# Kernel tuning notes

Hardware: AMD Instinct MI355X
Metric: run time of the kernel (lower is better)

## Reference

```python
import jax, jax.numpy as jnp
import numpy as np

B, S, E, H, DK = 2, 2048, 2048, 16, 128


def _make_freq_pos_enc(dim, max_seq_len):
    # matches torch freq_pos_enc: interleaved repeat '(f r)' with r=2
    inv_freq = 1.0 / (10000.0 ** (jnp.arange(0, dim, 2, dtype=jnp.float32) / dim))
    pos = jnp.arange(max_seq_len, dtype=jnp.float32)
    pe = pos[:, None] * inv_freq[None, :]          # [S, dim/2]
    return jnp.repeat(pe, 2, axis=-1)              # [S, dim], interleaved


def setup_inputs() -> dict:
    key = jax.random.key(0)
    ks = jax.random.split(key, 5)
    sc = 1.0 / np.sqrt(E)
    return {
        "x": jax.random.normal(ks[0], (B, S, E), jnp.float32),
        "wq": jax.random.normal(ks[1], (H * DK, E), jnp.float32) * sc,
        "wk": jax.random.normal(ks[2], (H * DK, E), jnp.float32) * sc,
        "wv": jax.random.normal(ks[3], (H * DK, E), jnp.float32) * sc,
        "wo": jax.random.normal(ks[4], (E, H * DK), jnp.float32) * sc,
        "freq_pos_enc": _make_freq_pos_enc(DK, S),
        "num_heads": H,
        "d_k": DK,
    }


def rotate_half(u):
    # interleaved pairs: (d r) with r=2 -> (-u2, u1) interleaved back
    shp = u.shape
    u = u.reshape(shp[:-1] + (shp[-1] // 2, 2))
    u1, u2 = u[..., 0], u[..., 1]
    return jnp.stack((-u2, u1), axis=-1).reshape(shp)


def reference(x, wq, wk, wv, wo, freq_pos_enc, num_heads, d_k):
    b, s, _ = x.shape

    def proj(w):  # [B,S,E] @ [E, H*DK] -> [B,H,S,DK]
        return (x @ w.T).reshape(b, s, num_heads, d_k).transpose(0, 2, 1, 3)

    q, k, v = proj(wq), proj(wk), proj(wv)

    pe = freq_pos_enc[:s]                           # [S, DK]
    cos, sin = jnp.cos(pe), jnp.sin(pe)
    rot = lambda u: u * cos + rotate_half(u) * sin  # broadcast over [B,H]
    q, k = rot(q), rot(k)

    scale = 1.0 / jnp.sqrt(jnp.asarray(d_k, x.dtype))
    scores = jnp.einsum('bhqd,bhkd->bhqk', q, k) * scale
    causal = jnp.tril(jnp.ones((s, s), bool))
    scores = jnp.where(causal, scores, jnp.finfo(scores.dtype).min)
    attn = jnp.einsum('bhqk,bhkd->bhqd', jax.nn.softmax(scores, axis=-1), v)

    out = attn.transpose(0, 2, 1, 3).reshape(b, s, num_heads * d_k)
    return out @ wo.T
```

## Files before the change

kernel.cpp:

```cpp
#include <hip/hip_runtime.h>
#include <hip/hip_bf16.h>

typedef __attribute__((ext_vector_type(8))) short bf16x8;
typedef __attribute__((ext_vector_type(4))) float f32x4;
typedef unsigned short u16;
typedef unsigned int u32;

#define B_ 2
#define S_ 2048
#define E_ 2048
#define H_ 16
#define DK_ 128
#define SCALE_ 0.08838834764831845f
#define THR_RAW_ 90.5f

#define MFMA16(a,b,c) __builtin_amdgcn_mfma_f32_16x16x32_bf16((a),(b),(c),0,0,0)
#define GLD16(g, l) __builtin_amdgcn_global_load_lds((const __attribute__((address_space(1))) void*)(g), (__attribute__((address_space(3))) void*)(l), 16, 0, 0)

__device__ __forceinline__ float b2f(short s) {
    u32 u = ((u32)(u16)s) << 16;
    float f; __builtin_memcpy(&f, &u, 4); return f;
}

__global__ void cast_f32_bf16(const float* __restrict__ in, __hip_bfloat16* __restrict__ out, int n4) {
    int i = blockIdx.x * blockDim.x + threadIdx.x;
    if (i >= n4) return;
    float4 v = ((const float4*)in)[i];
    __hip_bfloat16 ob[4] = {__float2bfloat16(v.x), __float2bfloat16(v.y),
                            __float2bfloat16(v.z), __float2bfloat16(v.w)};
    ushort4 u; __builtin_memcpy(&u, ob, 8);
    ((ushort4*)out)[i] = u;
}

__global__ void rope_kernel(__hip_bfloat16* __restrict__ q, __hip_bfloat16* __restrict__ k,
                            const float* __restrict__ pe) {
    const long i = ((long)blockIdx.x * blockDim.x + threadIdx.x) * 8;
    __hip_bfloat16* p = (blockIdx.y == 0 ? q : k) + i;
    const int d0 = (int)(i & (DK_ - 1));
    const int s  = (int)((i >> 7) & (S_ - 1));
    const float* pp = pe + (size_t)s * DK_ + d0;
    bf16x8 v = *(const bf16x8*)p;
    __hip_bfloat16 ob[8];
    #pragma unroll
    for (int j = 0; j < 4; ++j) {
        float ang = pp[2*j];
        float cs = cosf(ang), sn = sinf(ang);
        float e = b2f(v[2*j]), o = b2f(v[2*j+1]);
        ob[2*j]   = __float2bfloat16(e*cs - o*sn);
        ob[2*j+1] = __float2bfloat16(o*cs + e*sn);
    }
    bf16x8 w; __builtin_memcpy(&w, ob, 16);
    *(bf16x8*)p = w;
}

template<int OUTMODE>
__global__ __launch_bounds__(256, 2)
void gemm_bt(const __hip_bfloat16* __restrict__ A, const __hip_bfloat16* __restrict__ W,
             void* __restrict__ Cout, int M, int N, int K)
{
    __shared__ __align__(16) __hip_bfloat16 As[128 * 64];
    __shared__ __align__(16) __hip_bfloat16 Bs[128 * 64];
    const int tid = threadIdx.x;
    const int lane = tid & 63, wv = tid >> 6;
    const int wr = wv >> 1, wc = wv & 1;
    const int m0 = blockIdx.x * 128, n0 = blockIdx.y * 128;
    const int g = lane >> 4, c = lane & 15;

    f32x4 acc[4][4];
    #pragma unroll
    for (int i = 0; i < 4; ++i)
        #pragma unroll
        for (int j = 0; j < 4; ++j) acc[i][j] = f32x4{0.f, 0.f, 0.f, 0.f};

    for (int k0 = 0; k0 < K; k0 += 64) {
        __syncthreads();
        #pragma unroll
        for (int it = 0; it < 4; ++it) {
            int o = (it * 256 + tid) * 16;
            int row = o >> 7;
            int colb = (o ^ ((row & 7) << 4)) & 127;
            GLD16((const char*)(A + (size_t)(m0 + row) * K + k0) + colb, (char*)As + o);
            GLD16((const char*)(W + (size_t)(n0 + row) * K + k0) + colb, (char*)Bs + o);
        }
        __syncthreads();
        #pragma unroll
        for (int ks = 0; ks < 2; ++ks) {
            bf16x8 af[4], bfm[4];
            #pragma unroll
            for (int i = 0; i < 4; ++i) {
                int arow = wr * 64 + i * 16 + c;
                int ab = arow * 128 + ((ks * 64 + g * 16) ^ ((arow & 7) << 4));
                af[i] = *(const bf16x8*)((const char*)As + ab);
                int brow = wc * 64 + i * 16 + c;
                int bb = brow * 128 + ((ks * 64 + g * 16) ^ ((brow & 7) << 4));
                bfm[i] = *(const bf16x8*)((const char*)Bs + bb);
            }
            #pragma unroll
            for (int i = 0; i < 4; ++i)
                #pragma unroll
                for (int j = 0; j < 4; ++j)
                    acc[i][j] = MFMA16(af[i], bfm[j], acc[i][j]);
        }
    }

    #pragma unroll
    for (int i = 0; i < 4; ++i) {
        #pragma unroll
        for (int j = 0; j < 4; ++j) {
            #pragma unroll
            for (int r = 0; r < 4; ++r) {
                int m = m0 + wr * 64 + i * 16 + 4 * g + r;
                int n = n0 + wc * 64 + j * 16 + c;
                float v = acc[i][j][r];
                if (OUTMODE == 2) {
                    ((float*)Cout)[(size_t)m * N + n] = v;
                } else if (OUTMODE == 0) {
                    size_t a = ((size_t)((m >> 11) * 16 + (n >> 7)) * S_ + (m & (S_ - 1))) * DK_ + (n & (DK_ - 1));
                    ((__hip_bfloat16*)Cout)[a] = __float2bfloat16(v);
                } else {
                    size_t a = ((size_t)((n >> 11) * 16 + (m >> 7)) * DK_ + (m & (DK_ - 1))) * S_ + (n & (S_ - 1));
                    ((__hip_bfloat16*)Cout)[a] = __float2bfloat16(v);
                }
            }
        }
    }
}

__device__ __forceinline__ void stage_kv(const __hip_bfloat16* Kp, const __hip_bfloat16* Vp,
                                         char* ks, char* vs, int kv0, int tid) {
    #pragma unroll
    for (int it = 0; it < 4; ++it) {
        int o = (it * 256 + tid) * 16;
        int row = o >> 8;
        int cb = (o ^ ((row & 7) << 4)) & 255;
        GLD16((const char*)(Kp + (size_t)(kv0 + row) * DK_) + cb, ks + o);
    }
    #pragma unroll
    for (int it = 0; it < 4; ++it) {
        int o = (it * 256 + tid) * 16;
        int row = o >> 7;
        int cb = (o ^ ((row & 7) << 4)) & 127;
        GLD16((const char*)(Vp + (size_t)row * S_ + kv0) + cb, vs + o);
    }
}

__global__ __launch_bounds__(256, 2)
void attn_kernel(const __hip_bfloat16* __restrict__ Q,
                 const __hip_bfloat16* __restrict__ Kt,
                 const __hip_bfloat16* __restrict__ VT,
                 __hip_bfloat16* __restrict__ O)
{
    __shared__ __align__(16) __hip_bfloat16 Ks[2][64 * 128];
    __shared__ __align__(16) __hip_bfloat16 Vs[2][128 * 64];
    __shared__ __align__(16) __hip_bfloat16 Ps[4][16 * 72];

    const int tid = threadIdx.x, lane = tid & 63, w = tid >> 6;
    const int g = lane >> 4, c = lane & 15;
    const int bh = blockIdx.y, b = bh >> 4, h = bh & 15;
    const size_t base_bh = (size_t)bh * S_ * DK_;
    const __hip_bfloat16* Qp = Q + base_bh;
    const __hip_bfloat16* Kp = Kt + base_bh;
    const __hip_bfloat16* Vp = VT + base_bh;

    #pragma unroll 1
    for (int pass = 0; pass < 2; ++pass) {
        const int qt = pass ? (31 - (int)blockIdx.x) : (int)blockIdx.x;
        const int qw = qt * 64 + w * 16;
        const int ntiles = qt + 1;

        bf16x8 qf[4];
        #pragma unroll
        for (int ds = 0; ds < 4; ++ds)
            qf[ds] = *(const bf16x8*)(Qp + (size_t)(qw + c) * DK_ + ds * 32 + g * 8);

        f32x4 oacc[8];
        #pragma unroll
        for (int fd = 0; fd < 8; ++fd) oacc[fd] = f32x4{0.f, 0.f, 0.f, 0.f};
        float M[4], L[4];
        #pragma unroll
        for (int r = 0; r < 4; ++r) { M[r] = -1e30f; L[r] = 0.f; }

        stage_kv(Kp, Vp, (char*)Ks[0], (char*)Vs[0], 0, tid);
        __syncthreads();

        int cur = 0;
        for (int t = 0; t < ntiles; ++t) {
            const int kv0 = t * 64;
            if (t + 1 < ntiles)
                stage_kv(Kp, Vp, (char*)Ks[cur ^ 1], (char*)Vs[cur ^ 1], kv0 + 64, tid);

            const bool diag = (kv0 + 63 > qw);

            f32x4 sacc[4];
            #pragma unroll
            for (int f = 0; f < 4; ++f) sacc[f] = f32x4{0.f, 0.f, 0.f, 0.f};
            #pragma unroll
            for (int f = 0; f < 4; ++f) {
                #pragma unroll
                for (int ds = 0; ds < 4; ++ds) {
                    int krow = f * 16 + c;
                    int kbyt = krow * 256 + ((ds * 64 + g * 16) ^ ((krow & 7) << 4));
                    bf16x8 kf = *(const bf16x8*)((const char*)Ks[cur] + kbyt);
                    sacc[f] = MFMA16(qf[ds], kf, sacc[f]);
                }
            }

            float p[4][4];
            float mt[4] = {-1e30f, -1e30f, -1e30f, -1e30f};
            #pragma unroll
            for (int f = 0; f < 4; ++f)
                #pragma unroll
                for (int r = 0; r < 4; ++r) {
                    float v = sacc[f][r];
                    if (diag && (kv0 + f * 16 + c > qw + 4 * g + r)) v = -1e30f;
                    p[f][r] = v;
                    mt[r] = fmaxf(mt[r], v);
                }
            #pragma unroll
            for (int r = 0; r < 4; ++r) {
                float v = mt[r];
                v = fmaxf(v, __shfl_xor(v, 1));
                v = fmaxf(v, __shfl_xor(v, 2));
                v = fmaxf(v, __shfl_xor(v, 4));
                v = fmaxf(v, __shfl_xor(v, 8));
                mt[r] = v;
            }
            bool grow = (mt[0] > M[0] + THR_RAW_) || (mt[1] > M[1] + THR_RAW_) ||
                        (mt[2] > M[2] + THR_RAW_) || (mt[3] > M[3] + THR_RAW_);
            if (__any(grow)) {
                float al[4];
                #pragma unroll
                for (int r = 0; r < 4; ++r) {
                    float mn = fmaxf(M[r], mt[r]);
                    al[r] = __expf((M[r] - mn) * SCALE_);
                    M[r] = mn;
                    L[r] *= al[r];
                }
                #pragma unroll
                for (int fd = 0; fd < 8; ++fd)
                    #pragma unroll
                    for (int r = 0; r < 4; ++r) oacc[fd][r] *= al[r];
            }
            float ms[4];
            #pragma unroll
            for (int r = 0; r < 4; ++r) ms[r] = M[r] * SCALE_;
            float lt[4] = {0.f, 0.f, 0.f, 0.f};
            #pragma unroll
            for (int f = 0; f < 4; ++f)
                #pragma unroll
                for (int r = 0; r < 4; ++r) {
                    float e = __expf(__builtin_fmaf(p[f][r], SCALE_, -ms[r]));
                    lt[r] += e;
                    Ps[w][(4 * g + r) * 72 + f * 16 + c] = __float2bfloat16(e);
                }
            #pragma unroll
            for (int r = 0; r < 4; ++r) {
                float v = lt[r];
                v += __shfl_xor(v, 1);
                v += __shfl_xor(v, 2);
                v += __shfl_xor(v, 4);
                v += __shfl_xor(v, 8);
                L[r] += v;
            }

            #pragma unroll
            for (int ks2 = 0; ks2 < 2; ++ks2) {
                bf16x8 pf = *(const bf16x8*)&Ps[w][c * 72 + ks2 * 32 + g * 8];
                #pragma unroll
                for (int fd = 0; fd < 8; ++fd) {
                    int vrow = fd * 16 + c;
                    int vb = vrow * 128 + ((ks2 * 64 + g * 16) ^ ((vrow & 7) << 4));
                    bf16x8 vf = *(const bf16x8*)((const char*)Vs[cur] + vb);
                    oacc[fd] = MFMA16(pf, vf, oacc[fd]);
                }
            }
            __syncthreads();
            cur ^= 1;
        }

        float rl[4];
        #pragma unroll
        for (int r = 0; r < 4; ++r) rl[r] = 1.0f / L[r];
        #pragma unroll
        for (int fd = 0; fd < 8; ++fd) {
            #pragma unroll
            for (int r = 0; r < 4; ++r) {
                int s = qw + 4 * g + r;
                size_t a = ((size_t)(b * S_ + s)) * (H_ * DK_) + h * DK_ + fd * 16 + c;
                O[a] = __float2bfloat16(oacc[fd][r] * rl[r]);
            }
        }
    }
}

extern "C" void kernel_launch(void* const* d_in, const int* in_sizes, int n_in,
                              void* d_out, int out_size, void* d_ws, size_t ws_size,
                              hipStream_t stream) {
    const float* x  = (const float*)d_in[0];
    const float* wq = (const float*)d_in[1];
    const float* wk = (const float*)d_in[2];
    const float* wv = (const float*)d_in[3];
    const float* wo = (const float*)d_in[4];
    const float* pe = (const float*)d_in[5];
    float* out = (float*)d_out;

    const size_t XE = (size_t)B_ * S_ * E_;
    const size_t WE = (size_t)E_ * H_ * DK_;
    __hip_bfloat16* xb  = (__hip_bfloat16*)d_ws;
    __hip_bfloat16* wqb = xb + XE;
    __hip_bfloat16* wkb = wqb + WE;
    __hip_bfloat16* wvb = wkb + WE;
    __hip_bfloat16* wob = wvb + WE;
    __hip_bfloat16* qb  = wob + WE;
    __hip_bfloat16* kb  = qb + XE;
    __hip_bfloat16* vT  = kb + XE;
    __hip_bfloat16* at  = vT + XE;

    cast_f32_bf16<<<dim3((int)(XE / 4 / 256)), 256, 0, stream>>>(x,  xb,  (int)(XE / 4));
    cast_f32_bf16<<<dim3((int)(WE / 4 / 256)), 256, 0, stream>>>(wq, wqb, (int)(WE / 4));
    cast_f32_bf16<<<dim3((int)(WE / 4 / 256)), 256, 0, stream>>>(wk, wkb, (int)(WE / 4));
    cast_f32_bf16<<<dim3((int)(WE / 4 / 256)), 256, 0, stream>>>(wv, wvb, (int)(WE / 4));
    cast_f32_bf16<<<dim3((int)(WE / 4 / 256)), 256, 0, stream>>>(wo, wob, (int)(WE / 4));

    gemm_bt<0><<<dim3(32, 16), 256, 0, stream>>>(xb, wqb, qb, B_ * S_, H_ * DK_, E_);
    gemm_bt<0><<<dim3(32, 16), 256, 0, stream>>>(xb, wkb, kb, B_ * S_, H_ * DK_, E_);
    gemm_bt<1><<<dim3(16, 32), 256, 0, stream>>>(wvb, xb, vT, H_ * DK_, B_ * S_, E_);

    rope_kernel<<<dim3((int)(XE / 8 / 256), 2), 256, 0, stream>>>(qb, kb, pe);

    attn_kernel<<<dim3(16, B_ * H_), 256, 0, stream>>>(qb, kb, vT, at);

    gemm_bt<2><<<dim3(32, 16), 256, 0, stream>>>(at, wob, out, B_ * S_, E_, H_ * DK_);
}
```

Baseline: 299.6 us.

## Fuse QKV projections with RoPE epilogue, batch weight casts, remap attention grid

Merges the three Q/K/V projection GEMMs into a single launch and applies RoPE inside the Q/K epilogue using a precomputed cos/sin table and a lane shuffle to fetch the paired element. This removes the separate rope pass over Q and K. The four weight casts become one launch, and the V transpose store is vectorised to 4-element writes. The attention grid is flattened and remapped so that groups of heads are interleaved across blocks, which may improve L2 locality or load balance. In exchange the epilogue does extra global reads of the trig table, and the output GEMM is specialised to fp32 output.

```diff
diff --git a/kernel.cpp b/kernel.cpp
--- a/kernel.cpp
+++ b/kernel.cpp
@@ -32,31 +32,128 @@
     ((ushort4*)out)[i] = u;
 }
 
-__global__ void rope_kernel(__hip_bfloat16* __restrict__ q, __hip_bfloat16* __restrict__ k,
-                            const float* __restrict__ pe) {
-    const long i = ((long)blockIdx.x * blockDim.x + threadIdx.x) * 8;
-    __hip_bfloat16* p = (blockIdx.y == 0 ? q : k) + i;
-    const int d0 = (int)(i & (DK_ - 1));
-    const int s  = (int)((i >> 7) & (S_ - 1));
-    const float* pp = pe + (size_t)s * DK_ + d0;
-    bf16x8 v = *(const bf16x8*)p;
-    __hip_bfloat16 ob[8];
+__global__ void cast_w4(const float* __restrict__ w0, const float* __restrict__ w1,
+                        const float* __restrict__ w2, const float* __restrict__ w3,
+                        __hip_bfloat16* __restrict__ o0, __hip_bfloat16* __restrict__ o1,
+                        __hip_bfloat16* __restrict__ o2, __hip_bfloat16* __restrict__ o3,
+                        int n4) {
+    int i = blockIdx.x * blockDim.x + threadIdx.x;
+    if (i >= n4) return;
+    const float* in = blockIdx.y == 0 ? w0 : blockIdx.y == 1 ? w1 : blockIdx.y == 2 ? w2 : w3;
+    __hip_bfloat16* out = blockIdx.y == 0 ? o0 : blockIdx.y == 1 ? o1 : blockIdx.y == 2 ? o2 : o3;
+    float4 v = ((const float4*)in)[i];
+    __hip_bfloat16 ob[4] = {__float2bfloat16(v.x), __float2bfloat16(v.y),
+                            __float2bfloat16(v.z), __float2bfloat16(v.w)};
+    ushort4 u; __builtin_memcpy(&u, ob, 8);
+    ((ushort4*)out)[i] = u;
+}
+
+__global__ void trig_table(const float* __restrict__ pe, float* __restrict__ ct,
+                           float* __restrict__ st) {
+    int t = blockIdx.x * blockDim.x + threadIdx.x;
+    int s = t >> 6, d2 = t & 63;
+    float ang = pe[(size_t)s * DK_ + 2 * d2];
+    ct[t] = cosf(ang);
+    st[t] = sinf(ang);
+}
+
+__global__ __launch_bounds__(256, 2)
+void gemm_qkv(const __hip_bfloat16* __restrict__ X,
+              const __hip_bfloat16* __restrict__ WQ, const __hip_bfloat16* __restrict__ WK,
+              const __hip_bfloat16* __restrict__ WV,
+              __hip_bfloat16* __restrict__ Qo, __hip_bfloat16* __restrict__ Ko,
+              __hip_bfloat16* __restrict__ Vo,
+              const float* __restrict__ CT, const float* __restrict__ ST)
+{
+    __shared__ __align__(16) __hip_bfloat16 As[128 * 64];
+    __shared__ __align__(16) __hip_bfloat16 Bs[128 * 64];
+    const int tid = threadIdx.x;
+    const int lane = tid & 63, wv = tid >> 6;
+    const int wr = wv >> 1, wc = wv & 1;
+    const int which = blockIdx.y >> 4;
+    const __hip_bfloat16* W = which == 0 ? WQ : which == 1 ? WK : WV;
+    const int m0 = blockIdx.x * 128, n0 = (blockIdx.y & 15) * 128;
+    const int g = lane >> 4, c = lane & 15;
+    const int K = E_;
+
+    f32x4 acc[4][4];
     #pragma unroll
-    for (int j = 0; j < 4; ++j) {
-        float ang = pp[2*j];
-        float cs = cosf(ang), sn = sinf(ang);
-        float e = b2f(v[2*j]), o = b2f(v[2*j+1]);
-        ob[2*j]   = __float2bfloat16(e*cs - o*sn);
-        ob[2*j+1] = __float2bfloat16(o*cs + e*sn);
-    }
-    bf16x8 w; __builtin_memcpy(&w, ob, 16);
-    *(bf16x8*)p = w;
-}
-
-template<int OUTMODE>
+    for (int i = 0; i < 4; ++i)
+        #pragma unroll
+        for (int j = 0; j < 4; ++j) acc[i][j] = f32x4{0.f, 0.f, 0.f, 0.f};
+
+    for (int k0 = 0; k0 < K; k0 += 64) {
+        __syncthreads();
+        #pragma unroll
+        for (int it = 0; it < 4; ++it) {
+            int o = (it * 256 + tid) * 16;
+            int row = o >> 7;
+            int colb = (o ^ ((row & 7) << 4)) & 127;
+            GLD16((const char*)(X + (size_t)(m0 + row) * K + k0) + colb, (char*)As + o);
+            GLD16((const char*)(W + (size_t)(n0 + row) * K + k0) + colb, (char*)Bs + o);
+        }
+        __syncthreads();
+        #pragma unroll
+        for (int ks = 0; ks < 2; ++ks) {
+            bf16x8 af[4], bfm[4];
+            #pragma unroll
+            for (int i = 0; i < 4; ++i) {
+                int arow = wr * 64 + i * 16 + c;
+                int ab = arow * 128 + ((ks * 64 + g * 16) ^ ((arow & 7) << 4));
+                af[i] = *(const bf16x8*)((const char*)As + ab);
+                int brow = wc * 64 + i * 16 + c;
+                int bb = brow * 128 + ((ks * 64 + g * 16) ^ ((brow & 7) << 4));
+                bfm[i] = *(const bf16x8*)((const char*)Bs + bb);
+            }
+            #pragma unroll
+            for (int i = 0; i < 4; ++i)
+                #pragma unroll
+                for (int j = 0; j < 4; ++j)
+                    acc[i][j] = MFMA16(af[i], bfm[j], acc[i][j]);
+        }
+    }
+
+    if (which < 2) {
+        __hip_bfloat16* Cq = which == 0 ? Qo : Ko;
+        #pragma unroll
+        for (int i = 0; i < 4; ++i)
+            #pragma unroll
+            for (int j = 0; j < 4; ++j)
+                #pragma unroll
+                for (int r = 0; r < 4; ++r) {
+                    float v = acc[i][j][r];
+                    float vp = __shfl_xor(v, 1);
+                    int m = m0 + wr * 64 + i * 16 + 4 * g + r;
+                    int n = n0 + wc * 64 + j * 16 + c;
+                    int srow = m & (S_ - 1), d = n & (DK_ - 1);
+                    float cs = CT[srow * 64 + (d >> 1)];
+                    float sn = ST[srow * 64 + (d >> 1)];
+                    float o = (c & 1) ? __builtin_fmaf(v, cs, vp * sn)
+                                      : __builtin_fmaf(v, cs, -vp * sn);
+                    size_t a = ((size_t)((m >> 11) * 16 + (n >> 7)) * S_ + srow) * DK_ + d;
+                    Cq[a] = __float2bfloat16(o);
+                }
+    } else {
+        #pragma unroll
+        for (int i = 0; i < 4; ++i)
+            #pragma unroll
+            for (int j = 0; j < 4; ++j) {
+                int m = m0 + wr * 64 + i * 16 + 4 * g;
+                int n = n0 + wc * 64 + j * 16 + c;
+                int s0 = m & (S_ - 1), d = n & (DK_ - 1);
+                __hip_bfloat16 ob[4];
+                #pragma unroll
+                for (int r = 0; r < 4; ++r) ob[r] = __float2bfloat16(acc[i][j][r]);
+                ushort4 u; __builtin_memcpy(&u, ob, 8);
+                size_t a = ((size_t)((m >> 11) * 16 + (n >> 7)) * DK_ + d) * S_ + s0;
+                *(ushort4*)(Vo + a) = u;
+            }
+    }
+}
+
 __global__ __launch_bounds__(256, 2)
-void gemm_bt(const __hip_bfloat16* __restrict__ A, const __hip_bfloat16* __restrict__ W,
-             void* __restrict__ Cout, int M, int N, int K)
+void gemm_out(const __hip_bfloat16* __restrict__ A, const __hip_bfloat16* __restrict__ W,
+              float* __restrict__ Cout, int M, int N, int K)
 {
     __shared__ __align__(16) __hip_bfloat16 As[128 * 64];
     __shared__ __align__(16) __hip_bfloat16 Bs[128 * 64];
@@ -104,26 +201,15 @@
     }
 
     #pragma unroll
-    for (int i = 0; i < 4; ++i) {
-        #pragma unroll
-        for (int j = 0; j < 4; ++j) {
+    for (int i = 0; i < 4; ++i)
+        #pragma unroll
+        for (int j = 0; j < 4; ++j)
             #pragma unroll
             for (int r = 0; r < 4; ++r) {
                 int m = m0 + wr * 64 + i * 16 + 4 * g + r;
                 int n = n0 + wc * 64 + j * 16 + c;
-                float v = acc[i][j][r];
-                if (OUTMODE == 2) {
-                    ((float*)Cout)[(size_t)m * N + n] = v;
-                } else if (OUTMODE == 0) {
-                    size_t a = ((size_t)((m >> 11) * 16 + (n >> 7)) * S_ + (m & (S_ - 1))) * DK_ + (n & (DK_ - 1));
-                    ((__hip_bfloat16*)Cout)[a] = __float2bfloat16(v);
-                } else {
-                    size_t a = ((size_t)((n >> 11) * 16 + (m >> 7)) * DK_ + (m & (DK_ - 1))) * S_ + (n & (S_ - 1));
-                    ((__hip_bfloat16*)Cout)[a] = __float2bfloat16(v);
-                }
-            }
-        }
-    }
+                Cout[(size_t)m * N + n] = acc[i][j][r];
+            }
 }
 
 __device__ __forceinline__ void stage_kv(const __hip_bfloat16* Kp, const __hip_bfloat16* Vp,
@@ -156,7 +242,11 @@
 
     const int tid = threadIdx.x, lane = tid & 63, w = tid >> 6;
     const int g = lane >> 4, c = lane & 15;
-    const int bh = blockIdx.y, b = bh >> 4, h = bh & 15;
+    const int id = blockIdx.x;
+    const int slot = id & 7, jj = id >> 3;
+    const int bh = ((jj >> 4) << 3) | slot;
+    const int xq = jj & 15;
+    const int b = bh >> 4, h = bh & 15;
     const size_t base_bh = (size_t)bh * S_ * DK_;
     const __hip_bfloat16* Qp = Q + base_bh;
     const __hip_bfloat16* Kp = Kt + base_bh;
@@ -164,7 +254,7 @@
 
     #pragma unroll 1
     for (int pass = 0; pass < 2; ++pass) {
-        const int qt = pass ? (31 - (int)blockIdx.x) : (int)blockIdx.x;
+        const int qt = pass ? (31 - xq) : xq;
         const int qw = qt * 64 + w * 16;
         const int ntiles = qt + 1;
 
@@ -315,20 +405,18 @@
     __hip_bfloat16* kb  = qb + XE;
     __hip_bfloat16* vT  = kb + XE;
     __hip_bfloat16* at  = vT + XE;
-
-    cast_f32_bf16<<<dim3((int)(XE / 4 / 256)), 256, 0, stream>>>(x,  xb,  (int)(XE / 4));
-    cast_f32_bf16<<<dim3((int)(WE / 4 / 256)), 256, 0, stream>>>(wq, wqb, (int)(WE / 4));
-    cast_f32_bf16<<<dim3((int)(WE / 4 / 256)), 256, 0, stream>>>(wk, wkb, (int)(WE / 4));
-    cast_f32_bf16<<<dim3((int)(WE / 4 / 256)), 256, 0, stream>>>(wv, wvb, (int)(WE / 4));
-    cast_f32_bf16<<<dim3((int)(WE / 4 / 256)), 256, 0, stream>>>(wo, wob, (int)(WE / 4));
-
-    gemm_bt<0><<<dim3(32, 16), 256, 0, stream>>>(xb, wqb, qb, B_ * S_, H_ * DK_, E_);
-    gemm_bt<0><<<dim3(32, 16), 256, 0, stream>>>(xb, wkb, kb, B_ * S_, H_ * DK_, E_);
-    gemm_bt<1><<<dim3(16, 32), 256, 0, stream>>>(wvb, xb, vT, H_ * DK_, B_ * S_, E_);
-
-    rope_kernel<<<dim3((int)(XE / 8 / 256), 2), 256, 0, stream>>>(qb, kb, pe);
-
-    attn_kernel<<<dim3(16, B_ * H_), 256, 0, stream>>>(qb, kb, vT, at);
-
-    gemm_bt<2><<<dim3(32, 16), 256, 0, stream>>>(at, wob, out, B_ * S_, E_, H_ * DK_);
-}
+    float* ct = (float*)(at + XE);
+    float* st = ct + (size_t)S_ * 64;
+
+    cast_f32_bf16<<<dim3((int)(XE / 4 / 256)), 256, 0, stream>>>(x, xb, (int)(XE / 4));
+    cast_w4<<<dim3((int)(WE / 4 / 256), 4), 256, 0, stream>>>(wq, wk, wv, wo,
+                                                              wqb, wkb, wvb, wob,
+                                                              (int)(WE / 4));
+    trig_table<<<dim3(S_ * 64 / 256), 256, 0, stream>>>(pe, ct, st);
+
+    gemm_qkv<<<dim3(32, 48), 256, 0, stream>>>(xb, wqb, wkb, wvb, qb, kb, vT, ct, st);
+
+    attn_kernel<<<dim3(512), 256, 0, stream>>>(qb, kb, vT, at);
+
+    gemm_out<<<dim3(32, 16), 256, 0, stream>>>(at, wob, out, B_ * S_, E_, H_ * DK_);
+}
```

Result: faster. 273.4 us (-8.7%).
